# Kernel tuning notes

Measured on AMD Instinct MI355X. Metric: run time of the kernel, lower is better.

## Reference

```python
import jax, jax.numpy as jnp
import numpy as np
import math

B, S, HID = 2, 2048, 2048
NH, NKV = 32, 8
HD = HID // NH  # 64
N_REP = NH // NKV  # 4


def setup_inputs() -> dict:
    key = jax.random.key(0)
    ks = jax.random.split(key, 7)
    sc = 0.02
    return {
        "hidden_states": jax.random.normal(ks[0], (B, S, HID), jnp.float32),
        "cos": jax.random.normal(ks[1], (S, HD), jnp.float32),
        "sin": jax.random.normal(ks[2], (S, HD), jnp.float32),
        "wq": jax.random.normal(ks[3], (NH * HD, HID), jnp.float32) * sc,
        "wk": jax.random.normal(ks[4], (NKV * HD, HID), jnp.float32) * sc,
        "wv": jax.random.normal(ks[5], (NKV * HD, HID), jnp.float32) * sc,
        "wo": jax.random.normal(ks[6], (HID, NH * HD), jnp.float32) * sc,
    }


def _rotate_half(x):
    x1, x2 = jnp.split(x, 2, axis=-1)
    return jnp.concatenate([-x2, x1], axis=-1)


def _apply_rotary(q, k, cos, sin):
    # q: [B,S,NH,HD], k: [B,S,NKV,HD]; cos/sin: [S,HD] broadcast over batch, heads
    c = cos[None, :, None, :]
    s = sin[None, :, None, :]
    return q * c + _rotate_half(q) * s, k * c + _rotate_half(k) * s


def reference(hidden_states, cos, sin, wq, wk, wv, wo):
    x = hidden_states  # [B,S,HID]
    q = jnp.einsum('bsh,dh->bsd', x, wq).reshape(B, S, NH, HD)
    k = jnp.einsum('bsh,dh->bsd', x, wk).reshape(B, S, NKV, HD)
    v = jnp.einsum('bsh,dh->bsd', x, wv).reshape(B, S, NKV, HD)
    q, k = _apply_rotary(q, k, cos, sin)
    # repeat_kv: expand kv heads by N_REP -> [B,S,NH,HD]
    k = jnp.repeat(k, N_REP, axis=2)
    v = jnp.repeat(v, N_REP, axis=2)
    # [B,NH,S,HD]
    q = q.transpose(0, 2, 1, 3)
    k = k.transpose(0, 2, 1, 3)
    v = v.transpose(0, 2, 1, 3)
    scores = jnp.einsum('bhqd,bhkd->bhqk', q, k) / math.sqrt(HD)
    probs = jax.nn.softmax(scores.astype(jnp.float32), axis=-1).astype(q.dtype)
    out = jnp.einsum('bhqk,bhkd->bhqd', probs, v)
    out = out.transpose(0, 2, 1, 3).reshape(B, S, NH * HD)
    return jnp.einsum('bsd,hd->bsh', out, wo)
```

## Files before the change

kernel.cpp:

```cpp
#include <hip/hip_runtime.h>
#include <math.h>

#define B 2
#define S 2048
#define HID 2048
#define NH 32
#define NKV 8
#define HD 64
#define NREP 4

typedef __bf16 bf16_t;
typedef bf16_t bf16x8 __attribute__((ext_vector_type(8)));
typedef bf16_t bf16x2 __attribute__((ext_vector_type(2)));
typedef float floatx4 __attribute__((ext_vector_type(4)));

__device__ __forceinline__ void gld_lds16(const void* g, void* l) {
    __builtin_amdgcn_global_load_lds(
        (const __attribute__((address_space(1))) void*)g,
        (__attribute__((address_space(3))) void*)l, 16, 0, 0);
}

__device__ __forceinline__ int pack2(float a, float b) {
    bf16x2 v; v[0] = (bf16_t)a; v[1] = (bf16_t)b;
    return __builtin_bit_cast(int, v);
}

__global__ __launch_bounds__(256) void cast_all(const float* __restrict__ x,
                                                const float* __restrict__ wq,
                                                const float* __restrict__ wk,
                                                const float* __restrict__ wv,
                                                const float* __restrict__ wo,
                                                bf16_t* __restrict__ xb,
                                                bf16_t* __restrict__ wqkvb,
                                                bf16_t* __restrict__ wob) {
    int gid = blockIdx.x * 256 + threadIdx.x;
    const float* src; bf16_t* dst; int idx;
    if (gid < 1048576)      { src = x;  dst = xb;               idx = gid; }
    else if (gid < 1572864) { src = wq; dst = wqkvb;            idx = gid - 1048576; }
    else if (gid < 1703936) { src = wk; dst = wqkvb + 4194304;  idx = gid - 1572864; }
    else if (gid < 1835008) { src = wv; dst = wqkvb + 5242880;  idx = gid - 1703936; }
    else                    { src = wo; dst = wob;              idx = gid - 1835008; }
    size_t i = (size_t)idx * 8;
    float4 f0 = *(const float4*)(src + i);
    float4 f1 = *(const float4*)(src + i + 4);
    bf16x8 v;
    v[0] = (bf16_t)f0.x; v[1] = (bf16_t)f0.y; v[2] = (bf16_t)f0.z; v[3] = (bf16_t)f0.w;
    v[4] = (bf16_t)f1.x; v[5] = (bf16_t)f1.y; v[6] = (bf16_t)f1.z; v[7] = (bf16_t)f1.w;
    *(bf16x8*)(dst + i) = v;
}

#define TM 128
#define TN 128
#define BK 64

enum { MODE_QKV = 0, MODE_OUT = 2 };

template <int MODE>
__global__ __launch_bounds__(256) void gemm_mfma(const bf16_t* __restrict__ A,
                                                 const bf16_t* __restrict__ W,
                                                 void* __restrict__ outQ,
                                                 bf16_t* __restrict__ outK,
                                                 bf16_t* __restrict__ outV,
                                                 const float* __restrict__ cosp,
                                                 const float* __restrict__ sinp,
                                                 int M, int N, int K) {
    __shared__ __align__(16) bf16_t As[2 * TM * 32];
    __shared__ __align__(16) bf16_t Ws[2 * TN * 32];
    const int t    = threadIdx.x;
    const int wave = t >> 6, lane = t & 63;
    const int quad = lane >> 4, l16 = lane & 15;
    const int m0 = blockIdx.y * TM, n0 = blockIdx.x * TN;
    const int wm = (wave >> 1) * 64, wn = (wave & 1) * 64;

    floatx4 zero4 = {0.f, 0.f, 0.f, 0.f};
    floatx4 acc[4][4];
    #pragma unroll
    for (int i = 0; i < 4; ++i)
        #pragma unroll
        for (int j = 0; j < 4; ++j) acc[i][j] = zero4;

    const int r4 = t >> 2;
    const int c8 = (t & 3) * 8;
    const bf16_t* Arow = A + (size_t)(m0 + r4) * K + c8;
    const bf16_t* Wrow = W + (size_t)(n0 + r4) * K + c8;

    for (int k0 = 0; k0 < K; k0 += BK) {
        #pragma unroll
        for (int ks = 0; ks < 2; ++ks) {
            gld_lds16(Arow + k0 + ks * 32,          As + ks * 4096 + t * 8);
            gld_lds16(Arow + 64 * K + k0 + ks * 32, As + ks * 4096 + 2048 + t * 8);
            gld_lds16(Wrow + k0 + ks * 32,          Ws + ks * 4096 + t * 8);
            gld_lds16(Wrow + 64 * K + k0 + ks * 32, Ws + ks * 4096 + 2048 + t * 8);
        }
        __syncthreads();
        #pragma unroll
        for (int ks = 0; ks < 2; ++ks) {
            bf16x8 af[4], bfr[4];
            #pragma unroll
            for (int i = 0; i < 4; ++i)
                af[i] = *(bf16x8*)&As[ks * 4096 + (wm + i * 16 + l16) * 32 + quad * 8];
            #pragma unroll
            for (int j = 0; j < 4; ++j)
                bfr[j] = *(bf16x8*)&Ws[ks * 4096 + (wn + j * 16 + l16) * 32 + quad * 8];
            #pragma unroll
            for (int i = 0; i < 4; ++i)
                #pragma unroll
                for (int j = 0; j < 4; ++j)
                    acc[i][j] = __builtin_amdgcn_mfma_f32_16x16x32_bf16(af[i], bfr[j], acc[i][j], 0, 0, 0);
        }
        __syncthreads();
    }

    if constexpr (MODE == MODE_OUT) {
        float* C = (float*)outQ;
        #pragma unroll
        for (int i = 0; i < 4; ++i)
            #pragma unroll
            for (int r = 0; r < 4; ++r) {
                int row = m0 + wm + i * 16 + quad * 4 + r;
                #pragma unroll
                for (int j = 0; j < 4; ++j)
                    C[(size_t)row * N + n0 + wn + j * 16 + l16] = acc[i][j][r];
            }
    } else {
        const int hh = (n0 + wn) / 64;
        #pragma unroll
        for (int i = 0; i < 4; ++i)
            #pragma unroll
            for (int r = 0; r < 4; ++r) {
                int m = m0 + wm + i * 16 + quad * 4 + r;
                int b = m / S, s = m % S;
                if (hh < NH + NKV) {
                    bf16_t* base;
                    float sc;
                    if (hh < NH) {
                        base = (bf16_t*)outQ + ((size_t)(b * NH + hh) * S + s) * HD;
                        sc = 0.18033688011f;
                    } else {
                        base = outK + ((size_t)(b * NKV + (hh - NH)) * S + s) * HD;
                        sc = 1.0f;
                    }
                    #pragma unroll
                    for (int j = 0; j < 2; ++j) {
                        int d = j * 16 + l16;
                        float x1 = acc[i][j][r], x2 = acc[i][j + 2][r];
                        float c1 = cosp[s * HD + d],      s1 = sinp[s * HD + d];
                        float c2 = cosp[s * HD + d + 32], s2 = sinp[s * HD + d + 32];
                        base[d]      = (bf16_t)((x1 * c1 - x2 * s1) * sc);
                        base[d + 32] = (bf16_t)((x2 * c2 + x1 * s2) * sc);
                    }
                } else {
                    int kvh = hh - NH - NKV;
                    bf16_t* vb = outV + ((size_t)(b * NKV + kvh) * HD) * S + s;
                    #pragma unroll
                    for (int j = 0; j < 4; ++j)
                        vb[(size_t)(j * 16 + l16) * S] = (bf16_t)acc[i][j][r];
                }
            }
    }
}

#define PP 72
__global__ __launch_bounds__(128, 2) void attn_mfma(const bf16_t* __restrict__ Q,
                                                    const bf16_t* __restrict__ Kb,
                                                    const bf16_t* __restrict__ Vt,
                                                    bf16_t* __restrict__ Ob) {
    __shared__ __align__(16) bf16_t Ks[2 * 64 * 32];
    __shared__ __align__(16) bf16_t Vs[2 * 64 * 32];
    __shared__ __align__(16) bf16_t Pq[2 * 64 * PP];
    const int t    = threadIdx.x;
    const int wave = t >> 6, lane = t & 63;
    const int quad = lane >> 4, l16 = lane & 15;
    const int bh = blockIdx.y, b = bh / NH, h = bh % NH, kvh = h / NREP;
    const int q0 = blockIdx.x * 128;

    const bf16_t* qbase = Q + ((size_t)bh * S + q0 + wave * 64) * HD;
    const bf16_t* kbase = Kb + ((size_t)(b * NKV + kvh) * S) * HD;
    const bf16_t* vbase = Vt + (size_t)(b * NKV + kvh) * HD * S;
    bf16_t* Pqw = Pq + wave * 64 * PP;

    bf16x8 qf[4][2];
    #pragma unroll
    for (int qj = 0; qj < 4; ++qj)
        #pragma unroll
        for (int ks = 0; ks < 2; ++ks)
            qf[qj][ks] = *(const bf16x8*)(qbase + (size_t)(qj * 16 + l16) * HD + ks * 32 + quad * 8);

    floatx4 zero4 = {0.f, 0.f, 0.f, 0.f};
    floatx4 of[4][4];
    #pragma unroll
    for (int di = 0; di < 4; ++di)
        #pragma unroll
        for (int qj = 0; qj < 4; ++qj) of[di][qj] = zero4;
    float lsum[4] = {0.f, 0.f, 0.f, 0.f};

    const int r4 = t >> 2;
    const int c8 = (t & 3) * 8;

    for (int kt = 0; kt < S; kt += 64) {
        __syncthreads();
        #pragma unroll
        for (int ks = 0; ks < 2; ++ks) {
            gld_lds16(kbase + (size_t)(kt + r4) * HD + ks * 32 + c8,      Ks + ks * 2048 + t * 8);
            gld_lds16(kbase + (size_t)(kt + 32 + r4) * HD + ks * 32 + c8, Ks + ks * 2048 + 1024 + t * 8);
            gld_lds16(vbase + (size_t)r4 * S + kt + ks * 32 + c8,         Vs + ks * 2048 + t * 8);
            gld_lds16(vbase + (size_t)(32 + r4) * S + kt + ks * 32 + c8,  Vs + ks * 2048 + 1024 + t * 8);
        }
        __syncthreads();

        #pragma unroll
        for (int ki = 0; ki < 4; ++ki) {
            bf16x8 ka0 = *(bf16x8*)&Ks[0 * 2048 + (ki * 16 + l16) * 32 + quad * 8];
            bf16x8 ka1 = *(bf16x8*)&Ks[1 * 2048 + (ki * 16 + l16) * 32 + quad * 8];
            floatx4 sf[4];
            #pragma unroll
            for (int qj = 0; qj < 4; ++qj) sf[qj] = zero4;
            #pragma unroll
            for (int qj = 0; qj < 4; ++qj)
                sf[qj] = __builtin_amdgcn_mfma_f32_16x16x32_bf16(ka0, qf[qj][0], sf[qj], 0, 0, 0);
            #pragma unroll
            for (int qj = 0; qj < 4; ++qj)
                sf[qj] = __builtin_amdgcn_mfma_f32_16x16x32_bf16(ka1, qf[qj][1], sf[qj], 0, 0, 0);
            #pragma unroll
            for (int qj = 0; qj < 4; ++qj) {
                float p0 = __builtin_amdgcn_exp2f(sf[qj][0]);
                float p1 = __builtin_amdgcn_exp2f(sf[qj][1]);
                float p2 = __builtin_amdgcn_exp2f(sf[qj][2]);
                float p3 = __builtin_amdgcn_exp2f(sf[qj][3]);
                lsum[qj] += (p0 + p1) + (p2 + p3);
                int2 pk; pk.x = pack2(p0, p1); pk.y = pack2(p2, p3);
                *(int2*)&Pqw[(qj * 16 + l16) * PP + ki * 16 + quad * 4] = pk;
            }
        }

        #pragma unroll
        for (int ks = 0; ks < 2; ++ks) {
            bf16x8 pb[4], va[4];
            #pragma unroll
            for (int qj = 0; qj < 4; ++qj)
                pb[qj] = *(bf16x8*)&Pqw[(qj * 16 + l16) * PP + ks * 32 + quad * 8];
            #pragma unroll
            for (int di = 0; di < 4; ++di)
                va[di] = *(bf16x8*)&Vs[ks * 2048 + (di * 16 + l16) * 32 + quad * 8];
            #pragma unroll
            for (int di = 0; di < 4; ++di)
                #pragma unroll
                for (int qj = 0; qj < 4; ++qj)
                    of[di][qj] = __builtin_amdgcn_mfma_f32_16x16x32_bf16(va[di], pb[qj], of[di][qj], 0, 0, 0);
        }
    }

    #pragma unroll
    for (int qj = 0; qj < 4; ++qj) {
        float ls = lsum[qj];
        ls += __shfl_xor(ls, 16);
        ls += __shfl_xor(ls, 32);
        float inv = 1.f / ls;
        int q = q0 + wave * 64 + qj * 16 + l16;
        bf16_t* ob = Ob + ((size_t)(b * S + q)) * HID + h * HD;
        #pragma unroll
        for (int di = 0; di < 4; ++di) {
            int2 pk;
            pk.x = pack2(of[di][qj][0] * inv, of[di][qj][1] * inv);
            pk.y = pack2(of[di][qj][2] * inv, of[di][qj][3] * inv);
            *(int2*)(ob + di * 16 + quad * 4) = pk;
        }
    }
}

extern "C" void kernel_launch(void* const* d_in, const int* in_sizes, int n_in,
                              void* d_out, int out_size, void* d_ws, size_t ws_size,
                              hipStream_t stream) {
    const float* x    = (const float*)d_in[0];
    const float* cosp = (const float*)d_in[1];
    const float* sinp = (const float*)d_in[2];
    const float* wq   = (const float*)d_in[3];
    const float* wk   = (const float*)d_in[4];
    const float* wv   = (const float*)d_in[5];
    const float* wo   = (const float*)d_in[6];
    float* out = (float*)d_out;

    char* ws = (char*)d_ws;
    bf16_t* xb    = (bf16_t*)(ws);
    bf16_t* kb    = (bf16_t*)(ws + 16777216);
    bf16_t* vtb   = (bf16_t*)(ws + 20971520);
    bf16_t* wqkvb = (bf16_t*)(ws + 25165824);
    bf16_t* wob   = (bf16_t*)(ws + 37748736);
    bf16_t* attb  = (bf16_t*)(ws);
    bf16_t* qb    = (bf16_t*)d_out;

    const int M = B * S;

    cast_all<<<9216, 256, 0, stream>>>(x, wq, wk, wv, wo, xb, wqkvb, wob);

    gemm_mfma<MODE_QKV><<<dim3(3072 / TN, M / TM), 256, 0, stream>>>(
        xb, wqkvb, (void*)qb, kb, vtb, cosp, sinp, M, 3072, HID);

    attn_mfma<<<dim3(S / 128, B * NH), 128, 0, stream>>>(qb, kb, vtb, attb);

    gemm_mfma<MODE_OUT><<<dim3(2048 / TN, M / TM), 256, 0, stream>>>(
        attb, wob, (void*)out, nullptr, nullptr, nullptr, nullptr, M, 2048, HID);
}
```

Baseline: 315.0 us.

## Load K/V fragments directly from global, drop LDS staging and block barriers

```diff
diff --git a/kernel.cpp b/kernel.cpp
--- a/kernel.cpp
+++ b/kernel.cpp
@@ -161,22 +161,26 @@
 }
 
 #define PP 72
-__global__ __launch_bounds__(128, 2) void attn_mfma(const bf16_t* __restrict__ Q,
+__global__ __launch_bounds__(128, 3) void attn_mfma(const bf16_t* __restrict__ Q,
                                                     const bf16_t* __restrict__ Kb,
                                                     const bf16_t* __restrict__ Vt,
                                                     bf16_t* __restrict__ Ob) {
-    __shared__ __align__(16) bf16_t Ks[2 * 64 * 32];
-    __shared__ __align__(16) bf16_t Vs[2 * 64 * 32];
     __shared__ __align__(16) bf16_t Pq[2 * 64 * PP];
     const int t    = threadIdx.x;
     const int wave = t >> 6, lane = t & 63;
     const int quad = lane >> 4, l16 = lane & 15;
-    const int bh = blockIdx.y, b = bh / NH, h = bh % NH, kvh = h / NREP;
-    const int q0 = blockIdx.x * 128;
+
+    const int flat  = blockIdx.y * 16 + blockIdx.x;
+    const int local = flat >> 3;
+    const int combo = (flat & 7) * 2 + (local >> 6);
+    const int b = combo >> 3, kvh = combo & 7;
+    const int h  = kvh * NREP + ((local >> 4) & 3);
+    const int q0 = (local & 15) * 128;
+    const int bh = b * NH + h;
 
     const bf16_t* qbase = Q + ((size_t)bh * S + q0 + wave * 64) * HD;
-    const bf16_t* kbase = Kb + ((size_t)(b * NKV + kvh) * S) * HD;
-    const bf16_t* vbase = Vt + (size_t)(b * NKV + kvh) * HD * S;
+    const bf16_t* kfrag = Kb + ((size_t)(b * NKV + kvh) * S + l16) * HD + quad * 8;
+    const bf16_t* vfrag = Vt + ((size_t)(b * NKV + kvh) * HD + l16) * S + quad * 8;
     bf16_t* Pqw = Pq + wave * 64 * PP;
 
     bf16x8 qf[4][2];
@@ -194,33 +198,27 @@
         for (int qj = 0; qj < 4; ++qj) of[di][qj] = zero4;
     float lsum[4] = {0.f, 0.f, 0.f, 0.f};
 
-    const int r4 = t >> 2;
-    const int c8 = (t & 3) * 8;
-
     for (int kt = 0; kt < S; kt += 64) {
-        __syncthreads();
-        #pragma unroll
-        for (int ks = 0; ks < 2; ++ks) {
-            gld_lds16(kbase + (size_t)(kt + r4) * HD + ks * 32 + c8,      Ks + ks * 2048 + t * 8);
-            gld_lds16(kbase + (size_t)(kt + 32 + r4) * HD + ks * 32 + c8, Ks + ks * 2048 + 1024 + t * 8);
-            gld_lds16(vbase + (size_t)r4 * S + kt + ks * 32 + c8,         Vs + ks * 2048 + t * 8);
-            gld_lds16(vbase + (size_t)(32 + r4) * S + kt + ks * 32 + c8,  Vs + ks * 2048 + 1024 + t * 8);
-        }
-        __syncthreads();
+        bf16x8 ka[4][2];
+        #pragma unroll
+        for (int ki = 0; ki < 4; ++ki)
+            #pragma unroll
+            for (int ks = 0; ks < 2; ++ks)
+                ka[ki][ks] = *(const bf16x8*)(kfrag + (size_t)(kt + ki * 16) * HD + ks * 32);
 
         #pragma unroll
         for (int ki = 0; ki < 4; ++ki) {
-            bf16x8 ka0 = *(bf16x8*)&Ks[0 * 2048 + (ki * 16 + l16) * 32 + quad * 8];
-            bf16x8 ka1 = *(bf16x8*)&Ks[1 * 2048 + (ki * 16 + l16) * 32 + quad * 8];
             floatx4 sf[4];
             #pragma unroll
             for (int qj = 0; qj < 4; ++qj) sf[qj] = zero4;
+            __builtin_amdgcn_s_setprio(1);
             #pragma unroll
             for (int qj = 0; qj < 4; ++qj)
-                sf[qj] = __builtin_amdgcn_mfma_f32_16x16x32_bf16(ka0, qf[qj][0], sf[qj], 0, 0, 0);
+                sf[qj] = __builtin_amdgcn_mfma_f32_16x16x32_bf16(ka[ki][0], qf[qj][0], sf[qj], 0, 0, 0);
             #pragma unroll
             for (int qj = 0; qj < 4; ++qj)
-                sf[qj] = __builtin_amdgcn_mfma_f32_16x16x32_bf16(ka1, qf[qj][1], sf[qj], 0, 0, 0);
+                sf[qj] = __builtin_amdgcn_mfma_f32_16x16x32_bf16(ka[ki][1], qf[qj][1], sf[qj], 0, 0, 0);
+            __builtin_amdgcn_s_setprio(0);
             #pragma unroll
             for (int qj = 0; qj < 4; ++qj) {
                 float p0 = __builtin_amdgcn_exp2f(sf[qj][0]);
@@ -233,20 +231,26 @@
             }
         }
 
+        bf16x8 va[4][2];
+        #pragma unroll
+        for (int di = 0; di < 4; ++di)
+            #pragma unroll
+            for (int ks = 0; ks < 2; ++ks)
+                va[di][ks] = *(const bf16x8*)(vfrag + (size_t)(di * 16) * S + kt + ks * 32);
+
         #pragma unroll
         for (int ks = 0; ks < 2; ++ks) {
-            bf16x8 pb[4], va[4];
+            bf16x8 pb[4];
             #pragma unroll
             for (int qj = 0; qj < 4; ++qj)
                 pb[qj] = *(bf16x8*)&Pqw[(qj * 16 + l16) * PP + ks * 32 + quad * 8];
-            #pragma unroll
-            for (int di = 0; di < 4; ++di)
-                va[di] = *(bf16x8*)&Vs[ks * 2048 + (di * 16 + l16) * 32 + quad * 8];
+            __builtin_amdgcn_s_setprio(1);
             #pragma unroll
             for (int di = 0; di < 4; ++di)
                 #pragma unroll
                 for (int qj = 0; qj < 4; ++qj)
-                    of[di][qj] = __builtin_amdgcn_mfma_f32_16x16x32_bf16(va[di], pb[qj], of[di][qj], 0, 0, 0);
+                    of[di][qj] = __builtin_amdgcn_mfma_f32_16x16x32_bf16(va[di][ks], pb[qj], of[di][qj], 0, 0, 0);
+            __builtin_amdgcn_s_setprio(0);
         }
     }
 
```

After: 382.5 us. 21.4% more time.
